# Kernel tuning notes

Measured on AMD Instinct MI355X. Metric: run time of the kernel, lower is better.

Reference implementation:

```python
import jax, jax.numpy as jnp
import numpy as np

N = 100000   # node_num
E = 1000000  # edges per relation
DIN, DH, DOUT = 64, 32, 64  # in_dim, out_dim//2, out_dim
EPS = 1e-5


def setup_inputs() -> dict:
    key = jax.random.key(0)
    ks = jax.random.split(key, 32)
    def w(k, shape):
        fan_in = shape[0]
        return jax.random.normal(k, shape, dtype=jnp.float32) / np.sqrt(fan_in)
    inp = {}
    inp["init_emb"] = jax.random.normal(ks[0], (N, DIN), dtype=jnp.float32)
    inp["pos_edges"] = jax.random.randint(ks[1], (2, E), 0, N, dtype=jnp.int32)
    inp["neg_edges"] = jax.random.randint(ks[2], (2, E), 0, N, dtype=jnp.int32)
    # conv1: two relation layers + self-loop layer, 64 -> 32
    inp["c1_Wp"] = w(ks[3], (DIN, DH)); inp["c1_bp"] = jnp.zeros((DH,), jnp.float32)
    inp["c1_Wn"] = w(ks[4], (DIN, DH)); inp["c1_bn"] = jnp.zeros((DH,), jnp.float32)
    inp["c1_Ws"] = w(ks[5], (DIN, DH)); inp["c1_bs"] = jnp.zeros((DH,), jnp.float32)
    # conv2: 32 -> 32
    inp["c2_Wp"] = w(ks[6], (DH, DH)); inp["c2_bp"] = jnp.zeros((DH,), jnp.float32)
    inp["c2_Wn"] = w(ks[7], (DH, DH)); inp["c2_bn"] = jnp.zeros((DH,), jnp.float32)
    inp["c2_Ws"] = w(ks[8], (DH, DH)); inp["c2_bs"] = jnp.zeros((DH,), jnp.float32)
    # self.weight: Linear(32 -> 64)
    inp["w_W"] = w(ks[9], (DH, DOUT)); inp["w_b"] = jnp.zeros((DOUT,), jnp.float32)
    # readout MLP: Linear(64,64)+BN+ReLU, Linear(64,64)+BN+ReLU, Linear(64,1)
    inp["m1_W"] = w(ks[10], (DOUT, DOUT)); inp["m1_b"] = jnp.zeros((DOUT,), jnp.float32)
    inp["g1"] = jnp.ones((DOUT,), jnp.float32); inp["b1"] = jnp.zeros((DOUT,), jnp.float32)
    inp["m2_W"] = w(ks[11], (DOUT, DOUT)); inp["m2_b"] = jnp.zeros((DOUT,), jnp.float32)
    inp["g2"] = jnp.ones((DOUT,), jnp.float32); inp["b2"] = jnp.zeros((DOUT,), jnp.float32)
    inp["m3_W"] = w(ks[12], (DOUT, 1)); inp["m3_b"] = jnp.zeros((1,), jnp.float32)
    return inp


def _conv(x, pe, ne, Wp, bp, Wn, bn_, Ws, bs):
    # gather -> per-relation linear -> scatter_add, summed over 2 relations + self loop
    mp = x[pe[0]] @ Wp + bp                                  # [E, d_out]
    agg = jax.ops.segment_sum(mp, pe[1], num_segments=N)      # [N, d_out]
    mn = x[ne[0]] @ Wn + bn_
    agg = agg + jax.ops.segment_sum(mn, ne[1], num_segments=N)
    return agg + x @ Ws + bs


def _batchnorm(h, g, b):
    m = h.mean(axis=0)
    v = h.var(axis=0)
    return (h - m) * jax.lax.rsqrt(v + EPS) * g + b


def reference(init_emb, pos_edges, neg_edges,
              c1_Wp, c1_bp, c1_Wn, c1_bn, c1_Ws, c1_bs,
              c2_Wp, c2_bp, c2_Wn, c2_bn, c2_Ws, c2_bs,
              w_W, w_b, m1_W, m1_b, g1, b1, m2_W, m2_b, g2, b2, m3_W, m3_b):
    z = jnp.tanh(_conv(init_emb, pos_edges, neg_edges, c1_Wp, c1_bp, c1_Wn, c1_bn, c1_Ws, c1_bs))
    z = jnp.tanh(_conv(z, pos_edges, neg_edges, c2_Wp, c2_bp, c2_Wn, c2_bn, c2_Ws, c2_bs))
    z = jnp.tanh(z @ w_W + w_b)                               # [N, 64]
    h = jax.nn.relu(_batchnorm(z @ m1_W + m1_b, g1, b1))      # dropout p=0.2 disabled (eval)
    h = jax.nn.relu(_batchnorm(h @ m2_W + m2_b, g2, b2))
    prob = jax.nn.sigmoid(h @ m3_W + m3_b)                    # [N, 1]
    return (z, prob)
```

## Files before the change

### kernel.cpp

```cpp
#include <hip/hip_runtime.h>
#include <cstdint>
#include <cstddef>

#define NN 100000
#define EE 1000000
#define EPSF 1e-5f
#define NBUK 391
#define NBUK2 (2*NBUK)
#define NBLK 256
#define EPB 7813
#define GSB 782
#define GTILES ((NN + 63) / 64)
#define MLP_GRID 512

typedef __attribute__((ext_vector_type(8))) short bf16x8;
typedef __attribute__((ext_vector_type(4))) float f32x4;

__device__ __forceinline__ void fatomic(float* p, float v) { unsafeAtomicAdd(p, v); }

__device__ __forceinline__ short f2bf(float f) {
    unsigned u = __float_as_uint(f);
    u += 0x7FFF + ((u >> 16) & 1);
    return (short)(u >> 16);
}

__device__ __forceinline__ void edge_of(const int* __restrict__ pe, const int* __restrict__ ne,
                                        int s, int& src, int& dst, int& bucket) {
    if (s < EE) { src = pe[s]; dst = pe[EE + s]; bucket = dst >> 8; }
    else        { src = ne[s - EE]; dst = ne[s]; bucket = NBUK + (dst >> 8); }
}

__global__ __launch_bounds__(256) void k_hist(const int* __restrict__ pe,
                                              const int* __restrict__ ne,
                                              int* __restrict__ hist) {
    __shared__ int lh[NBUK2];
    for (int i = threadIdx.x; i < NBUK2; i += 256) lh[i] = 0;
    __syncthreads();
    int start = blockIdx.x * EPB, end = min(start + EPB, 2 * EE);
    for (int s = start + threadIdx.x; s < end; s += 256) {
        int src, dst, bucket;
        edge_of(pe, ne, s, src, dst, bucket);
        atomicAdd(&lh[bucket], 1);
    }
    __syncthreads();
    for (int i = threadIdx.x; i < NBUK2; i += 256)
        hist[i * NBLK + blockIdx.x] = lh[i];
}

__global__ __launch_bounds__(256) void k_gscan1(const int* __restrict__ in,
                                                int* __restrict__ out,
                                                int* __restrict__ partials) {
    int i = blockIdx.x * 256 + threadIdx.x;
    int v = in[i];
    __shared__ int s[256];
    s[threadIdx.x] = v;
    __syncthreads();
    for (int off = 1; off < 256; off <<= 1) {
        int u = (threadIdx.x >= off) ? s[threadIdx.x - off] : 0;
        __syncthreads();
        s[threadIdx.x] += u;
        __syncthreads();
    }
    out[i] = s[threadIdx.x] - v;
    if (threadIdx.x == 255) partials[blockIdx.x] = s[255];
}

__global__ __launch_bounds__(1024) void k_gscan2(int* __restrict__ partials) {
    __shared__ int s[1024];
    int v = (threadIdx.x < GSB) ? partials[threadIdx.x] : 0;
    s[threadIdx.x] = v;
    __syncthreads();
    for (int off = 1; off < 1024; off <<= 1) {
        int u = (threadIdx.x >= off) ? s[threadIdx.x - off] : 0;
        __syncthreads();
        s[threadIdx.x] += u;
        __syncthreads();
    }
    if (threadIdx.x < GSB) partials[threadIdx.x] = s[threadIdx.x] - v;
}

__global__ __launch_bounds__(256) void k_gscan3(const int* __restrict__ partials,
                                                int* __restrict__ out) {
    out[blockIdx.x * 256 + threadIdx.x] += partials[blockIdx.x];
}

__global__ __launch_bounds__(256) void k_binscatter(const int* __restrict__ pe,
                                                    const int* __restrict__ ne,
                                                    const int* __restrict__ soff,
                                                    unsigned long long* __restrict__ staging) {
    __shared__ int cur[NBUK2];
    for (int i = threadIdx.x; i < NBUK2; i += 256)
        cur[i] = soff[i * NBLK + blockIdx.x];
    __syncthreads();
    int start = blockIdx.x * EPB, end = min(start + EPB, 2 * EE);
    for (int s = start + threadIdx.x; s < end; s += 256) {
        int src, dst, bucket;
        edge_of(pe, ne, s, src, dst, bucket);
        int pos = atomicAdd(&cur[bucket], 1);
        staging[pos] = ((unsigned long long)(unsigned)dst << 32) | (unsigned)src;
    }
}

__global__ __launch_bounds__(256) void k_local(const unsigned long long* __restrict__ staging,
                                               const int* __restrict__ soff,
                                               int* __restrict__ rpP,
                                               int* __restrict__ rpN,
                                               int* __restrict__ csrAll) {
    int bucket = blockIdx.x;
    int rel = bucket >= NBUK;
    int nodeBase = (bucket - rel * NBUK) << 8;
    int bstart = soff[bucket * NBLK];
    int bend = (bucket == NBUK2 - 1) ? 2 * EE : soff[(bucket + 1) * NBLK];
    int tid = threadIdx.x;
    __shared__ int deg[256], sc[256];
    deg[tid] = 0;
    __syncthreads();
    for (int i = bstart + tid; i < bend; i += 256) {
        int d = (int)(staging[i] >> 32) & 255;
        atomicAdd(&deg[d], 1);
    }
    __syncthreads();
    int dv = deg[tid];
    sc[tid] = dv;
    __syncthreads();
    for (int off = 1; off < 256; off <<= 1) {
        int u = (tid >= off) ? sc[tid - off] : 0;
        __syncthreads();
        sc[tid] += u;
        __syncthreads();
    }
    int lrp = sc[tid] - dv;
    int nCount = min(256, NN - nodeBase);
    int relbase = rel ? EE : 0;
    if (tid < nCount) (rel ? rpN : rpP)[nodeBase + tid] = bstart - relbase + lrp;
    if (bucket == NBUK - 1 && tid == 0) rpP[NN] = EE;
    if (bucket == NBUK2 - 1 && tid == 0) rpN[NN] = EE;
    deg[tid] = lrp;
    __syncthreads();
    for (int i = bstart + tid; i < bend; i += 256) {
        unsigned long long v = staging[i];
        int d = (int)(v >> 32) & 255;
        int src = (int)(v & 0xffffffffu);
        int slot = atomicAdd(&deg[d], 1);
        csrAll[bstart + slot] = src;
    }
}

__global__ __launch_bounds__(192) __attribute__((amdgpu_waves_per_eu(2, 4)))
void k_xf1(const float* __restrict__ x,
           const float* __restrict__ Wp,
           const float* __restrict__ Wn,
           const float* __restrict__ Ws,
           float* __restrict__ xp,
           float* __restrict__ xn,
           float* __restrict__ xs) {
    __shared__ float sx[64 * 64];
    int base = blockIdx.x * 64;
    int tid = threadIdx.x;
    int wvm = tid >> 6;
    int l = tid & 63;
    int j = l & 31;
    int half = l >> 5;
    for (int idx = tid; idx < 1024; idx += 192) {
        int row = idx >> 4, f = idx & 15;
        int n = base + row;
        float4 v = (n < NN) ? *(const float4*)&x[(size_t)n * 64 + f * 4]
                            : make_float4(0.f, 0.f, 0.f, 0.f);
        *(float4*)&sx[row * 64 + f * 4] = v;
    }
    const float* W = (wvm == 0) ? Wp : (wvm == 1) ? Wn : Ws;
    float* outm = (wvm == 0) ? xp : (wvm == 1) ? xn : xs;
    float w[64];
    #pragma unroll
    for (int k = 0; k < 64; k++) w[k] = W[k * 32 + j];
    __syncthreads();
    #pragma unroll 1
    for (int i = 0; i < 32; i++) {
        int nl = 2 * i + half;
        int n = base + nl;
        float a0 = 0.f, a1 = 0.f, a2 = 0.f, a3 = 0.f;
        #pragma unroll
        for (int q = 0; q < 16; q++) {
            float4 xv = *(const float4*)&sx[nl * 64 + q * 4];
            a0 += xv.x * w[q * 4 + 0];
            a1 += xv.y * w[q * 4 + 1];
            a2 += xv.z * w[q * 4 + 2];
            a3 += xv.w * w[q * 4 + 3];
        }
        if (n < NN) outm[(size_t)n * 32 + j] = (a0 + a1) + (a2 + a3);
    }
}

__global__ __launch_bounds__(192) __attribute__((amdgpu_waves_per_eu(2, 4)))
void k_xf2(const float* __restrict__ z,
           const float* __restrict__ Wp,
           const float* __restrict__ Wn,
           const float* __restrict__ Ws,
           float* __restrict__ xp,
           float* __restrict__ xn,
           float* __restrict__ xs) {
    __shared__ float sx[64 * 32];
    int base = blockIdx.x * 64;
    int tid = threadIdx.x;
    int wvm = tid >> 6;
    int l = tid & 63;
    int j = l & 31;
    int half = l >> 5;
    for (int idx = tid; idx < 512; idx += 192) {
        int row = idx >> 3, f = idx & 7;
        int n = base + row;
        float4 v = (n < NN) ? *(const float4*)&z[(size_t)n * 32 + f * 4]
                            : make_float4(0.f, 0.f, 0.f, 0.f);
        *(float4*)&sx[row * 32 + f * 4] = v;
    }
    const float* W = (wvm == 0) ? Wp : (wvm == 1) ? Wn : Ws;
    float* outm = (wvm == 0) ? xp : (wvm == 1) ? xn : xs;
    float w[32];
    #pragma unroll
    for (int k = 0; k < 32; k++) w[k] = W[k * 32 + j];
    __syncthreads();
    #pragma unroll 1
    for (int i = 0; i < 32; i++) {
        int nl = 2 * i + half;
        int n = base + nl;
        float a0 = 0.f, a1 = 0.f, a2 = 0.f, a3 = 0.f;
        #pragma unroll
        for (int q = 0; q < 8; q++) {
            float4 xv = *(const float4*)&sx[nl * 32 + q * 4];
            a0 += xv.x * w[q * 4 + 0];
            a1 += xv.y * w[q * 4 + 1];
            a2 += xv.z * w[q * 4 + 2];
            a3 += xv.w * w[q * 4 + 3];
        }
        if (n < NN) outm[(size_t)n * 32 + j] = (a0 + a1) + (a2 + a3);
    }
}

__device__ __forceinline__ float pull_rel(const float* __restrict__ xsrc,
                                          const int* __restrict__ csr,
                                          int b0, int b1, int j, float acc) {
    for (int base = b0; base < b1; base += 32) {
        int rem = b1 - base;
        int cnt = min(rem, 32);
        int idx = (j < rem) ? csr[base + j] : 0;
        int i = 0;
        for (; i + 4 <= cnt; i += 4) {
            int s0 = __shfl(idx, i, 32);
            int s1 = __shfl(idx, i + 1, 32);
            int s2 = __shfl(idx, i + 2, 32);
            int s3 = __shfl(idx, i + 3, 32);
            float v0 = xsrc[(size_t)s0 * 32 + j];
            float v1 = xsrc[(size_t)s1 * 32 + j];
            float v2 = xsrc[(size_t)s2 * 32 + j];
            float v3 = xsrc[(size_t)s3 * 32 + j];
            acc += v0; acc += v1; acc += v2; acc += v3;
        }
        for (; i < cnt; i++) {
            int s = __shfl(idx, i, 32);
            acc += xsrc[(size_t)s * 32 + j];
        }
    }
    return acc;
}

__global__ __launch_bounds__(256) void k_pull(const float* __restrict__ xp,
                                              const float* __restrict__ xn,
                                              const float* __restrict__ xs,
                                              const int* __restrict__ rpP,
                                              const int* __restrict__ csrP,
                                              const int* __restrict__ rpN,
                                              const int* __restrict__ csrN,
                                              const float* __restrict__ bp,
                                              const float* __restrict__ bn,
                                              const float* __restrict__ bs,
                                              float* __restrict__ out) {
    int j = threadIdx.x & 31;
    int hw = (blockIdx.x * 256 + threadIdx.x) >> 5;
    const int nhw = (2048 * 256) >> 5;
    float bpj = bp[j], bnj = bn[j], bsj = bs[j];
    for (int n = hw; n < NN; n += nhw) {
        int p0 = rpP[n], p1 = rpP[n + 1];
        int n0 = rpN[n], n1 = rpN[n + 1];
        float acc = xs[(size_t)n * 32 + j] + bsj
                  + (float)(p1 - p0) * bpj + (float)(n1 - n0) * bnj;
        acc = pull_rel(xp, csrP, p0, p1, j, acc);
        acc = pull_rel(xn, csrN, n0, n1, j, acc);
        out[(size_t)n * 32 + j] = tanhf(acc);
    }
}

__global__ __launch_bounds__(256) __attribute__((amdgpu_waves_per_eu(2, 4)))
void k_wlin(const float* __restrict__ z2,
            const float* __restrict__ Wl,
            const float* __restrict__ bl,
            float* __restrict__ z) {
    __shared__ float sx[64 * 32];
    int base = blockIdx.x * 64;
    int tid = threadIdx.x;
    int lane = tid & 63;
    int wv = tid >> 6;
    {
        int row = tid >> 2, c4 = tid & 3;
        int n = base + row;
        #pragma unroll
        for (int m = 0; m < 2; m++) {
            int f = c4 + 4 * m;
            float4 v = (n < NN) ? *(const float4*)&z2[(size_t)n * 32 + f * 4]
                                : make_float4(0.f, 0.f, 0.f, 0.f);
            *(float4*)&sx[row * 32 + f * 4] = v;
        }
    }
    float wl[32];
    #pragma unroll
    for (int k = 0; k < 32; k++) wl[k] = Wl[k * 64 + lane];
    float blj = bl[lane];
    __syncthreads();
    #pragma unroll 1
    for (int i = 0; i < 16; i++) {
        int nl = i * 4 + wv;
        int n = base + nl;
        float a0 = 0.f, a1c = 0.f, a2 = 0.f, a3 = 0.f;
        #pragma unroll
        for (int q = 0; q < 8; q++) {
            float4 xv = *(const float4*)&sx[nl * 32 + q * 4];
            a0 += xv.x * wl[q * 4 + 0];
            a1c += xv.y * wl[q * 4 + 1];
            a2 += xv.z * wl[q * 4 + 2];
            a3 += xv.w * wl[q * 4 + 3];
        }
        if (n < NN) z[(size_t)n * 64 + lane] = tanhf(blj + ((a0 + a1c) + (a2 + a3)));
    }
}

__global__ __launch_bounds__(256) __attribute__((amdgpu_waves_per_eu(2, 4)))
void k_mlp(const float* __restrict__ in,
           const float* __restrict__ a1,
           const float* __restrict__ c1,
           int doBN,
           const float* __restrict__ W,
           const float* __restrict__ b,
           float* __restrict__ out,
           float* __restrict__ colsum,
           float* __restrict__ colsq) {
    __shared__ float scol[64], ssq[64];
    int tid = threadIdx.x;
    if (tid < 64) { scol[tid] = 0.f; ssq[tid] = 0.f; }
    int wv = tid >> 6;
    int l = tid & 63;
    int r16 = l & 15, kg = l >> 4;

    bf16x8 bf[4][2];
    #pragma unroll
    for (int ct = 0; ct < 4; ct++)
        #pragma unroll
        for (int h = 0; h < 2; h++)
            #pragma unroll
            for (int i = 0; i < 8; i++) {
                int k = h * 32 + ((i < 4) ? kg * 4 + i : 16 + kg * 4 + (i - 4));
                bf[ct][h][i] = f2bf(W[k * 64 + ct * 16 + r16]);
            }
    float bj[4];
    #pragma unroll
    for (int ct = 0; ct < 4; ct++) bj[ct] = b[ct * 16 + r16];

    float av0[2][4], cv0[2][4], av1[2][4], cv1[2][4];
    #pragma unroll
    for (int h = 0; h < 2; h++) {
        int k0 = h * 32 + kg * 4;
        int k1 = h * 32 + 16 + kg * 4;
        #pragma unroll
        for (int i = 0; i < 4; i++) {
            av0[h][i] = doBN ? a1[k0 + i] : 1.f;
            cv0[h][i] = doBN ? c1[k0 + i] : 0.f;
            av1[h][i] = doBN ? a1[k1 + i] : 1.f;
            cv1[h][i] = doBN ? c1[k1 + i] : 0.f;
        }
    }

    float lsum[4] = {0.f, 0.f, 0.f, 0.f}, lsq[4] = {0.f, 0.f, 0.f, 0.f};

    for (int tile = blockIdx.x; tile < GTILES; tile += MLP_GRID) {
        int base = tile * 64;
        int arow = base + wv * 16 + r16;
        bool rv = arow < NN;
        bf16x8 af[2];
        #pragma unroll
        for (int h = 0; h < 2; h++) {
            int k0 = h * 32 + kg * 4;
            int k1 = h * 32 + 16 + kg * 4;
            float4 v0 = rv ? *(const float4*)&in[(size_t)arow * 64 + k0]
                           : make_float4(0.f, 0.f, 0.f, 0.f);
            float4 v1 = rv ? *(const float4*)&in[(size_t)arow * 64 + k1]
                           : make_float4(0.f, 0.f, 0.f, 0.f);
            if (doBN) {
                v0.x = fmaxf(v0.x * av0[h][0] + cv0[h][0], 0.f);
                v0.y = fmaxf(v0.y * av0[h][1] + cv0[h][1], 0.f);
                v0.z = fmaxf(v0.z * av0[h][2] + cv0[h][2], 0.f);
                v0.w = fmaxf(v0.w * av0[h][3] + cv0[h][3], 0.f);
                v1.x = fmaxf(v1.x * av1[h][0] + cv1[h][0], 0.f);
                v1.y = fmaxf(v1.y * av1[h][1] + cv1[h][1], 0.f);
                v1.z = fmaxf(v1.z * av1[h][2] + cv1[h][2], 0.f);
                v1.w = fmaxf(v1.w * av1[h][3] + cv1[h][3], 0.f);
            }
            af[h][0] = f2bf(v0.x); af[h][1] = f2bf(v0.y);
            af[h][2] = f2bf(v0.z); af[h][3] = f2bf(v0.w);
            af[h][4] = f2bf(v1.x); af[h][5] = f2bf(v1.y);
            af[h][6] = f2bf(v1.z); af[h][7] = f2bf(v1.w);
        }

        f32x4 acc[4];
        #pragma unroll
        for (int ct = 0; ct < 4; ct++) { acc[ct][0] = 0.f; acc[ct][1] = 0.f; acc[ct][2] = 0.f; acc[ct][3] = 0.f; }
        #pragma unroll
        for (int h = 0; h < 2; h++)
            #pragma unroll
            for (int ct = 0; ct < 4; ct++)
                acc[ct] = __builtin_amdgcn_mfma_f32_16x16x32_bf16(af[h], bf[ct][h], acc[ct], 0, 0, 0);

        #pragma unroll
        for (int ct = 0; ct < 4; ct++) {
            int col = ct * 16 + r16;
            #pragma unroll
            for (int i = 0; i < 4; i++) {
                int orow = base + wv * 16 + kg * 4 + i;
                if (orow < NN) {
                    float s = acc[ct][i] + bj[ct];
                    out[(size_t)orow * 64 + col] = s;
                    lsum[ct] += s; lsq[ct] += s * s;
                }
            }
        }
    }

    __syncthreads();
    #pragma unroll
    for (int ct = 0; ct < 4; ct++) {
        atomicAdd(&scol[ct * 16 + r16], lsum[ct]);
        atomicAdd(&ssq[ct * 16 + r16], lsq[ct]);
    }
    __syncthreads();
    if (tid < 64) {
        fatomic(&colsum[tid], scol[tid]);
        fatomic(&colsq[tid], ssq[tid]);
    }
}

__global__ void k_bnstats(const float* __restrict__ colsum, const float* __restrict__ colsq,
                          const float* __restrict__ g, const float* __restrict__ beta,
                          float* __restrict__ a, float* __restrict__ c) {
    int j = threadIdx.x;
    if (j < 64) {
        float m = colsum[j] * (1.f / NN);
        float v = colsq[j] * (1.f / NN) - m * m;
        float aj = g[j] * rsqrtf(v + EPSF);
        a[j] = aj;
        c[j] = beta[j] - m * aj;
    }
}

__global__ __launch_bounds__(256) void k_mlp3(const float* __restrict__ t2,
                                              const float* __restrict__ a2,
                                              const float* __restrict__ c2,
                                              const float* __restrict__ W3,
                                              const float* __restrict__ b3,
                                              float* __restrict__ prob) {
    int j = threadIdx.x & 63;
    int r = threadIdx.x >> 6;
    float aj = a2[j], cj = c2[j], wj = W3[j], bb = b3[0];
    for (int n = blockIdx.x * 4 + r; n < NN; n += 2048 * 4) {
        float h = fmaxf(t2[(size_t)n * 64 + j] * aj + cj, 0.f) * wj;
        #pragma unroll
        for (int off = 32; off > 0; off >>= 1) h += __shfl_xor(h, off, 64);
        if (j == 0) prob[n] = 1.f / (1.f + expf(-(h + bb)));
    }
}

extern "C" void kernel_launch(void* const* d_in, const int* in_sizes, int n_in,
                              void* d_out, int out_size, void* d_ws, size_t ws_size,
                              hipStream_t stream) {
    const float* init_emb = (const float*)d_in[0];
    const int* pe = (const int*)d_in[1];
    const int* ne = (const int*)d_in[2];
    const float* c1_Wp = (const float*)d_in[3];  const float* c1_bp = (const float*)d_in[4];
    const float* c1_Wn = (const float*)d_in[5];  const float* c1_bn = (const float*)d_in[6];
    const float* c1_Ws = (const float*)d_in[7];  const float* c1_bs = (const float*)d_in[8];
    const float* c2_Wp = (const float*)d_in[9];  const float* c2_bp = (const float*)d_in[10];
    const float* c2_Wn = (const float*)d_in[11]; const float* c2_bn = (const float*)d_in[12];
    const float* c2_Ws = (const float*)d_in[13]; const float* c2_bs = (const float*)d_in[14];
    const float* w_W = (const float*)d_in[15];   const float* w_b = (const float*)d_in[16];
    const float* m1_W = (const float*)d_in[17];  const float* m1_b = (const float*)d_in[18];
    const float* g1 = (const float*)d_in[19];    const float* b1 = (const float*)d_in[20];
    const float* m2_W = (const float*)d_in[21];  const float* m2_b = (const float*)d_in[22];
    const float* g2 = (const float*)d_in[23];    const float* b2 = (const float*)d_in[24];
    const float* m3_W = (const float*)d_in[25];  const float* m3_b = (const float*)d_in[26];

    size_t off = 0;
    auto alloc = [&](size_t bytes) -> void* {
        void* r = (char*)d_ws + off;
        off += (bytes + 255) & ~(size_t)255;
        return r;
    };
    float* sums = (float*)alloc(256 * 4);
    size_t zero_bytes = off;
    size_t csr_region = off;
    int*   hist = (int*)alloc((size_t)NBUK2 * NBLK * 4);
    int*   soff = (int*)alloc((size_t)NBUK2 * NBLK * 4);
    int*   part = (int*)alloc((size_t)1024 * 4);
    unsigned long long* staging = (unsigned long long*)alloc((size_t)2 * EE * 8);
    int*   csrAll = (int*)alloc((size_t)2 * EE * 4);
    int*   rpP  = (int*)alloc((size_t)(NN + 1) * 4);
    int*   rpN  = (int*)alloc((size_t)(NN + 1) * 4);
    float* R1   = (float*)alloc((size_t)NN * 96 * 4);
    float* z1   = (float*)alloc((size_t)NN * 32 * 4);
    float* z2   = (float*)alloc((size_t)NN * 32 * 4);
    float* abc  = (float*)alloc(256 * 4);

    int* csrP = csrAll;
    int* csrN = csrAll + (size_t)EE;
    float* xp = R1;
    float* xn = R1 + (size_t)NN * 32;
    float* xs = R1 + (size_t)NN * 64;
    float* t1 = R1;
    float* t2 = (float*)((char*)d_ws + csr_region);

    float* z_out = (float*)d_out;
    float* prob  = (float*)d_out + (size_t)NN * 64;

    hipMemsetAsync(d_ws, 0, zero_bytes, stream);

    k_hist<<<NBLK, 256, 0, stream>>>(pe, ne, hist);
    k_gscan1<<<GSB, 256, 0, stream>>>(hist, soff, part);
    k_gscan2<<<1, 1024, 0, stream>>>(part);
    k_gscan3<<<GSB, 256, 0, stream>>>(part, soff);
    k_binscatter<<<NBLK, 256, 0, stream>>>(pe, ne, soff, staging);
    k_local<<<NBUK2, 256, 0, stream>>>(staging, soff, rpP, rpN, csrAll);

    k_xf1<<<GTILES, 192, 0, stream>>>(init_emb, c1_Wp, c1_Wn, c1_Ws, xp, xn, xs);
    k_pull<<<2048, 256, 0, stream>>>(xp, xn, xs, rpP, csrP, rpN, csrN, c1_bp, c1_bn, c1_bs, z1);
    k_xf2<<<GTILES, 192, 0, stream>>>(z1, c2_Wp, c2_Wn, c2_Ws, xp, xn, xs);
    k_pull<<<2048, 256, 0, stream>>>(xp, xn, xs, rpP, csrP, rpN, csrN, c2_bp, c2_bn, c2_bs, z2);
    k_wlin<<<GTILES, 256, 0, stream>>>(z2, w_W, w_b, z_out);
    k_mlp<<<MLP_GRID, 256, 0, stream>>>(z_out, nullptr, nullptr, 0, m1_W, m1_b, t1, sums + 0, sums + 64);
    k_bnstats<<<1, 64, 0, stream>>>(sums + 0, sums + 64, g1, b1, abc + 0, abc + 64);
    k_mlp<<<MLP_GRID, 256, 0, stream>>>(t1, abc + 0, abc + 64, 1, m2_W, m2_b, t2, sums + 128, sums + 192);
    k_bnstats<<<1, 64, 0, stream>>>(sums + 128, sums + 192, g2, b2, abc + 128, abc + 192);
    k_mlp3<<<2048, 256, 0, stream>>>(t2, abc + 128, abc + 192, m3_W, m3_b, prob);
}
```

Before: 301.7 us.

## Use split-bf16 MFMA for per-relation node transforms in both conv layers

The two node-transform kernels are rewritten from scalar FP32 FMA loops over an LDS tile into bf16 MFMA 16x16x32 matrix ops. Inputs and weights are split into hi and lo bf16 parts and combined with three MFMAs to stay close to FP32 accuracy. A persistent grid-stride loop over 16-row tiles replaces one block per 64 rows, and the LDS staging is dropped in favour of direct float4 loads. The split adds conversion work and drops the lo*lo term, so results differ slightly from exact FP32.

```diff
diff --git a/kernel.cpp b/kernel.cpp
--- a/kernel.cpp
+++ b/kernel.cpp
@@ -12,6 +12,8 @@
 #define GSB 782
 #define GTILES ((NN + 63) / 64)
 #define MLP_GRID 512
+#define XFT (NN / 16)
+#define XF_GRID 512
 
 typedef __attribute__((ext_vector_type(8))) short bf16x8;
 typedef __attribute__((ext_vector_type(4))) float f32x4;
@@ -22,6 +24,21 @@
     unsigned u = __float_as_uint(f);
     u += 0x7FFF + ((u >> 16) & 1);
     return (short)(u >> 16);
+}
+__device__ __forceinline__ float bf2f(short s) {
+    return __uint_as_float(((unsigned)(unsigned short)s) << 16);
+}
+__device__ __forceinline__ void split8(const float4 v0, const float4 v1, bf16x8& hi, bf16x8& lo) {
+    float a[8] = {v0.x, v0.y, v0.z, v0.w, v1.x, v1.y, v1.z, v1.w};
+    #pragma unroll
+    for (int i = 0; i < 8; i++) {
+        short h = f2bf(a[i]);
+        hi[i] = h;
+        lo[i] = f2bf(a[i] - bf2f(h));
+    }
+}
+__device__ __forceinline__ int kmap(int kg, int i) {
+    return (i < 4) ? kg * 4 + i : 16 + kg * 4 + (i - 4);
 }
 
 __device__ __forceinline__ void edge_of(const int* __restrict__ pe, const int* __restrict__ ne,
@@ -154,40 +171,55 @@
            float* __restrict__ xp,
            float* __restrict__ xn,
            float* __restrict__ xs) {
-    __shared__ float sx[64 * 64];
-    int base = blockIdx.x * 64;
     int tid = threadIdx.x;
     int wvm = tid >> 6;
     int l = tid & 63;
-    int j = l & 31;
-    int half = l >> 5;
-    for (int idx = tid; idx < 1024; idx += 192) {
-        int row = idx >> 4, f = idx & 15;
-        int n = base + row;
-        float4 v = (n < NN) ? *(const float4*)&x[(size_t)n * 64 + f * 4]
-                            : make_float4(0.f, 0.f, 0.f, 0.f);
-        *(float4*)&sx[row * 64 + f * 4] = v;
-    }
+    int r16 = l & 15, kg = l >> 4;
     const float* W = (wvm == 0) ? Wp : (wvm == 1) ? Wn : Ws;
     float* outm = (wvm == 0) ? xp : (wvm == 1) ? xn : xs;
-    float w[64];
-    #pragma unroll
-    for (int k = 0; k < 64; k++) w[k] = W[k * 32 + j];
-    __syncthreads();
-    #pragma unroll 1
-    for (int i = 0; i < 32; i++) {
-        int nl = 2 * i + half;
-        int n = base + nl;
-        float a0 = 0.f, a1 = 0.f, a2 = 0.f, a3 = 0.f;
-        #pragma unroll
-        for (int q = 0; q < 16; q++) {
-            float4 xv = *(const float4*)&sx[nl * 64 + q * 4];
-            a0 += xv.x * w[q * 4 + 0];
-            a1 += xv.y * w[q * 4 + 1];
-            a2 += xv.z * w[q * 4 + 2];
-            a3 += xv.w * w[q * 4 + 3];
-        }
-        if (n < NN) outm[(size_t)n * 32 + j] = (a0 + a1) + (a2 + a3);
+
+    bf16x8 bh[2][2], bl[2][2];
+    #pragma unroll
+    for (int ct = 0; ct < 2; ct++)
+        #pragma unroll
+        for (int h = 0; h < 2; h++)
+            #pragma unroll
+            for (int i = 0; i < 8; i++) {
+                int k = h * 32 + kmap(kg, i);
+                float w = W[k * 32 + ct * 16 + r16];
+                short hi = f2bf(w);
+                bh[ct][h][i] = hi;
+                bl[ct][h][i] = f2bf(w - bf2f(hi));
+            }
+
+    for (int tile = blockIdx.x; tile < XFT; tile += XF_GRID) {
+        int rbase = tile * 16;
+        int arow = rbase + r16;
+        bf16x8 ah[2], al[2];
+        #pragma unroll
+        for (int h = 0; h < 2; h++) {
+            int k0 = h * 32 + kg * 4;
+            int k1 = h * 32 + 16 + kg * 4;
+            float4 v0 = *(const float4*)&x[(size_t)arow * 64 + k0];
+            float4 v1 = *(const float4*)&x[(size_t)arow * 64 + k1];
+            split8(v0, v1, ah[h], al[h]);
+        }
+        f32x4 acc[2];
+        #pragma unroll
+        for (int ct = 0; ct < 2; ct++) { acc[ct][0] = 0.f; acc[ct][1] = 0.f; acc[ct][2] = 0.f; acc[ct][3] = 0.f; }
+        #pragma unroll
+        for (int h = 0; h < 2; h++)
+            #pragma unroll
+            for (int ct = 0; ct < 2; ct++) {
+                acc[ct] = __builtin_amdgcn_mfma_f32_16x16x32_bf16(ah[h], bh[ct][h], acc[ct], 0, 0, 0);
+                acc[ct] = __builtin_amdgcn_mfma_f32_16x16x32_bf16(al[h], bh[ct][h], acc[ct], 0, 0, 0);
+                acc[ct] = __builtin_amdgcn_mfma_f32_16x16x32_bf16(ah[h], bl[ct][h], acc[ct], 0, 0, 0);
+            }
+        #pragma unroll
+        for (int ct = 0; ct < 2; ct++)
+            #pragma unroll
+            for (int i = 0; i < 4; i++)
+                outm[(size_t)(rbase + kg * 4 + i) * 32 + ct * 16 + r16] = acc[ct][i];
     }
 }
 
@@ -199,40 +231,46 @@
            float* __restrict__ xp,
            float* __restrict__ xn,
            float* __restrict__ xs) {
-    __shared__ float sx[64 * 32];
-    int base = blockIdx.x * 64;
     int tid = threadIdx.x;
     int wvm = tid >> 6;
     int l = tid & 63;
-    int j = l & 31;
-    int half = l >> 5;
-    for (int idx = tid; idx < 512; idx += 192) {
-        int row = idx >> 3, f = idx & 7;
-        int n = base + row;
-        float4 v = (n < NN) ? *(const float4*)&z[(size_t)n * 32 + f * 4]
-                            : make_float4(0.f, 0.f, 0.f, 0.f);
-        *(float4*)&sx[row * 32 + f * 4] = v;
-    }
+    int r16 = l & 15, kg = l >> 4;
     const float* W = (wvm == 0) ? Wp : (wvm == 1) ? Wn : Ws;
     float* outm = (wvm == 0) ? xp : (wvm == 1) ? xn : xs;
-    float w[32];
-    #pragma unroll
-    for (int k = 0; k < 32; k++) w[k] = W[k * 32 + j];
-    __syncthreads();
-    #pragma unroll 1
-    for (int i = 0; i < 32; i++) {
-        int nl = 2 * i + half;
-        int n = base + nl;
-        float a0 = 0.f, a1 = 0.f, a2 = 0.f, a3 = 0.f;
-        #pragma unroll
-        for (int q = 0; q < 8; q++) {
-            float4 xv = *(const float4*)&sx[nl * 32 + q * 4];
-            a0 += xv.x * w[q * 4 + 0];
-            a1 += xv.y * w[q * 4 + 1];
-            a2 += xv.z * w[q * 4 + 2];
-            a3 += xv.w * w[q * 4 + 3];
-        }
-        if (n < NN) outm[(size_t)n * 32 + j] = (a0 + a1) + (a2 + a3);
+
+    bf16x8 bh[2], bl[2];
+    #pragma unroll
+    for (int ct = 0; ct < 2; ct++)
+        #pragma unroll
+        for (int i = 0; i < 8; i++) {
+            int k = kmap(kg, i);
+            float w = W[k * 32 + ct * 16 + r16];
+            short hi = f2bf(w);
+            bh[ct][i] = hi;
+            bl[ct][i] = f2bf(w - bf2f(hi));
+        }
+
+    for (int tile = blockIdx.x; tile < XFT; tile += XF_GRID) {
+        int rbase = tile * 16;
+        int arow = rbase + r16;
+        float4 v0 = *(const float4*)&z[(size_t)arow * 32 + kg * 4];
+        float4 v1 = *(const float4*)&z[(size_t)arow * 32 + 16 + kg * 4];
+        bf16x8 ah, al;
+        split8(v0, v1, ah, al);
+        f32x4 acc[2];
+        #pragma unroll
+        for (int ct = 0; ct < 2; ct++) { acc[ct][0] = 0.f; acc[ct][1] = 0.f; acc[ct][2] = 0.f; acc[ct][3] = 0.f; }
+        #pragma unroll
+        for (int ct = 0; ct < 2; ct++) {
+            acc[ct] = __builtin_amdgcn_mfma_f32_16x16x32_bf16(ah, bh[ct], acc[ct], 0, 0, 0);
+            acc[ct] = __builtin_amdgcn_mfma_f32_16x16x32_bf16(al, bh[ct], acc[ct], 0, 0, 0);
+            acc[ct] = __builtin_amdgcn_mfma_f32_16x16x32_bf16(ah, bl[ct], acc[ct], 0, 0, 0);
+        }
+        #pragma unroll
+        for (int ct = 0; ct < 2; ct++)
+            #pragma unroll
+            for (int i = 0; i < 4; i++)
+                outm[(size_t)(rbase + kg * 4 + i) * 32 + ct * 16 + r16] = acc[ct][i];
     }
 }
 
@@ -356,7 +394,7 @@
         for (int h = 0; h < 2; h++)
             #pragma unroll
             for (int i = 0; i < 8; i++) {
-                int k = h * 32 + ((i < 4) ? kg * 4 + i : 16 + kg * 4 + (i - 4));
+                int k = h * 32 + kmap(kg, i);
                 bf[ct][h][i] = f2bf(W[k * 64 + ct * 16 + r16]);
             }
     float bj[4];
@@ -535,9 +573,9 @@
     k_binscatter<<<NBLK, 256, 0, stream>>>(pe, ne, soff, staging);
     k_local<<<NBUK2, 256, 0, stream>>>(staging, soff, rpP, rpN, csrAll);
 
-    k_xf1<<<GTILES, 192, 0, stream>>>(init_emb, c1_Wp, c1_Wn, c1_Ws, xp, xn, xs);
+    k_xf1<<<XF_GRID, 192, 0, stream>>>(init_emb, c1_Wp, c1_Wn, c1_Ws, xp, xn, xs);
     k_pull<<<2048, 256, 0, stream>>>(xp, xn, xs, rpP, csrP, rpN, csrN, c1_bp, c1_bn, c1_bs, z1);
-    k_xf2<<<GTILES, 192, 0, stream>>>(z1, c2_Wp, c2_Wn, c2_Ws, xp, xn, xs);
+    k_xf2<<<XF_GRID, 192, 0, stream>>>(z1, c2_Wp, c2_Wn, c2_Ws, xp, xn, xs);
     k_pull<<<2048, 256, 0, stream>>>(xp, xn, xs, rpP, csrP, rpN, csrN, c2_bp, c2_bn, c2_bs, z2);
     k_wlin<<<GTILES, 256, 0, stream>>>(z2, w_W, w_b, z_out);
     k_mlp<<<MLP_GRID, 256, 0, stream>>>(z_out, nullptr, nullptr, 0, m1_W, m1_b, t1, sums + 0, sums + 64);
```

Result: faster. 268.5 us (-11.0%).
